# Kernel optimization log

Measured on AMD Instinct MI355X. Metric: run time of the kernel, lower is better.

Reference implementation:

```python
import jax, jax.numpy as jnp
import numpy as np

B, S, H, E, K, F = 2, 2048, 1024, 8, 2, 4096


def setup_inputs() -> dict:
    key = jax.random.key(0)
    ks = jax.random.split(key, 6)
    scale = 0.02
    return {
        "x": jax.random.normal(ks[0], (B, S, H), dtype=jnp.float32),
        "Wg": jax.random.normal(ks[1], (H, E), dtype=jnp.float32) * scale,
        "bg": jnp.zeros((E,), dtype=jnp.float32),
        "W1": jax.random.normal(ks[2], (E, H, F), dtype=jnp.float32) * scale,  # gate proj per expert
        "W3": jax.random.normal(ks[3], (E, H, F), dtype=jnp.float32) * scale,  # up proj per expert
        "W2": jax.random.normal(ks[4], (E, F, H), dtype=jnp.float32) * scale,  # down proj per expert
    }


def reference(x, Wg, bg, W1, W3, W2):
    # --- gating: softmax -> top-k -> renormalize ---
    probs = jax.nn.softmax(jnp.einsum("bsh,he->bse", x, Wg) + bg, axis=-1)  # [B,S,E]
    topw, topi = jax.lax.top_k(probs, K)                                     # [B,S,K]
    topw = topw / jnp.sum(topw, axis=-1, keepdims=True)
    # combine weights per expert: sum over k slots of weight where index==e
    cw = jnp.sum(jax.nn.one_hot(topi, E, dtype=x.dtype) * topw[..., None], axis=-2)  # [B,S,E]

    # --- dense grouped SwiGLU experts; cw==0 zeroes out non-selected tokens,
    # which is mathematically identical to the original masked gather/scatter loop ---
    g = jnp.einsum("bsh,ehf->bsef", x, W1)            # [B,S,E,F]
    u = jnp.einsum("bsh,ehf->bsef", x, W3)            # [B,S,E,F]
    h = jax.nn.silu(g) * u                             # [B,S,E,F]
    out = jnp.einsum("bsef,efh,bse->bsh", h, W2, cw)  # weighted combine
    return out
```

## Files before the change

kernel.cpp:

```cpp
#include <hip/hip_runtime.h>
#include <hip/hip_bf16.h>
#include <math.h>

#define HD 1024
#define FD 4096
#define NE 8
#define CAP 4096

typedef __attribute__((ext_vector_type(8))) short short8;
typedef __attribute__((ext_vector_type(4))) float f32x4;

__device__ inline unsigned short f2b(float f) {
    union { float f; unsigned u; } v; v.f = f;
    unsigned r = v.u + 0x7FFF + ((v.u >> 16) & 1);
    return (unsigned short)(r >> 16);
}

__device__ inline void gll16(const void* g, void* l) {
    __builtin_amdgcn_global_load_lds(
        (const __attribute__((address_space(1))) unsigned int*)g,
        (__attribute__((address_space(3))) unsigned int*)l, 16, 0, 0);
}

__global__ __launch_bounds__(256) void convx_kernel(const float* __restrict__ x,
                                                    unsigned short* __restrict__ xbf)
{
    int i = blockIdx.x * 256 + threadIdx.x;
    float4 v = *(const float4*)(x + (size_t)i * 4);
    ushort4 b; b.x = f2b(v.x); b.y = f2b(v.y); b.z = f2b(v.z); b.w = f2b(v.w);
    *(ushort4*)(xbf + (size_t)i * 4) = b;
}

__global__ __launch_bounds__(256) void transpose_kernel(const float* __restrict__ in,
                                                        unsigned short* __restrict__ out,
                                                        int R, int C)
{
    __shared__ unsigned short Ls[64 * 72];
    int t = threadIdx.x;
    int r0 = blockIdx.x * 64, c0 = blockIdx.y * 64;
    const float* ip = in + (size_t)blockIdx.z * R * C;
    unsigned short* op = out + (size_t)blockIdx.z * R * C;

    int rl = t >> 4, c4 = (t & 15) * 4;
#pragma unroll
    for (int p = 0; p < 4; p++) {
        int r = p * 16 + rl;
        float4 v = *(const float4*)(ip + (size_t)(r0 + r) * C + c0 + c4);
        Ls[(c4 + 0) * 72 + r] = f2b(v.x);
        Ls[(c4 + 1) * 72 + r] = f2b(v.y);
        Ls[(c4 + 2) * 72 + r] = f2b(v.z);
        Ls[(c4 + 3) * 72 + r] = f2b(v.w);
    }
    __syncthreads();
    int c = t >> 2, j2 = (t & 3) * 2;
#pragma unroll
    for (int q = 0; q < 2; q++) {
        int j = j2 + q;
        uint4 v = *(const uint4*)&Ls[c * 72 + j * 8];
        *(uint4*)(op + (size_t)(c0 + c) * R + r0 + j * 8) = v;
    }
}

__global__ __launch_bounds__(256) void gate_kernel(
    const float* __restrict__ x, const float* __restrict__ Wg,
    const float* __restrict__ bg, int* __restrict__ cnt,
    int* __restrict__ btok, float* __restrict__ bw,
    int* __restrict__ tokSlot, int T)
{
    int wave = threadIdx.x >> 6;
    int lane = threadIdx.x & 63;
    int t = blockIdx.x * 4 + wave;
    if (t >= T) return;

    float part[NE];
#pragma unroll
    for (int e = 0; e < NE; e++) part[e] = 0.f;
    const float* xr = x + (size_t)t * HD;
#pragma unroll 4
    for (int j = 0; j < 16; j++) {
        int h = lane + 64 * j;
        float xv = xr[h];
        const float* wr = Wg + h * NE;
#pragma unroll
        for (int e = 0; e < NE; e++) part[e] += xv * wr[e];
    }
#pragma unroll
    for (int e = 0; e < NE; e++) {
        float v = part[e];
        for (int off = 32; off >= 1; off >>= 1) v += __shfl_xor(v, off, 64);
        part[e] = v;
    }
    if (lane == 0) {
        float lg[NE];
#pragma unroll
        for (int e = 0; e < NE; e++) lg[e] = part[e] + bg[e];
        int i0 = 0;
        for (int e = 1; e < NE; e++) if (lg[e] > lg[i0]) i0 = e;
        int i1 = -1;
        for (int e = 0; e < NE; e++) {
            if (e == i0) continue;
            if (i1 < 0 || lg[e] > lg[i1]) i1 = e;
        }
        float e1 = expf(lg[i1] - lg[i0]);
        float s = 1.0f + e1;
        float w0 = 1.0f / s, w1 = e1 / s;
        int p0 = atomicAdd(&cnt[i0], 1);
        int p1 = atomicAdd(&cnt[i1], 1);
        btok[i0 * CAP + p0] = t; bw[i0 * CAP + p0] = w0;
        btok[i1 * CAP + p1] = t; bw[i1 * CAP + p1] = w1;
        tokSlot[t * 2 + 0] = i0 * CAP + p0;
        tokSlot[t * 2 + 1] = i1 * CAP + p1;
    }
}

__global__ void scan_kernel(const int* __restrict__ cnt, int* __restrict__ offs)
{
    if (threadIdx.x == 0) {
        int acc = 0;
        for (int e = 0; e < NE; e++) { offs[e] = acc; acc += cnt[e]; }
    }
}

__global__ __launch_bounds__(256, 2) void gemm1_kernel(
    const unsigned short* __restrict__ xbf, const unsigned short* __restrict__ Wt1,
    const unsigned short* __restrict__ Wt3, const int* __restrict__ btok,
    const int* __restrict__ cnt, const int* __restrict__ offs,
    unsigned short* __restrict__ h_buf)
{
    int e = blockIdx.z;
    int ne = cnt[e];
    int m0 = blockIdx.y * 128;
    if (m0 >= ne) return;
    int f0 = blockIdx.x * 128;

    __shared__ unsigned short As[3][4096];
    __shared__ unsigned short B1s[3][4096];
    __shared__ unsigned short B3s[3][4096];

    int tid = threadIdx.x;
    int lane = tid & 63;
    int w = tid >> 6;
    int wm = (w >> 1) * 64, wn = (w & 1) * 64;
    int l15 = lane & 15, quad = lane >> 4;

    const unsigned short* W1e = Wt1 + (size_t)e * HD * FD;
    const unsigned short* W3e = Wt3 + (size_t)e * HD * FD;

    const unsigned short* aA[2];
    const unsigned short* aB1[2];
    const unsigned short* aB3[2];
    int dst[2];
#pragma unroll
    for (int q = 0; q < 2; q++) {
        int row = q * 64 + lane;
        dst[q] = w * 1024 + q * 512;
        int ridx = m0 + row; if (ridx >= ne) ridx = ne - 1;
        int tok = btok[e * CAP + ridx];
        aA[q]  = xbf + (size_t)tok * HD + w * 8;
        aB1[q] = W1e + (size_t)(f0 + row) * HD + w * 8;
        aB3[q] = W3e + (size_t)(f0 + row) * HD + w * 8;
    }

    int aoff[4], boff[4];
#pragma unroll
    for (int i = 0; i < 4; i++) {
        aoff[i] = quad * 1024 + (wm + i * 16 + l15) * 8;
        boff[i] = quad * 1024 + (wn + i * 16 + l15) * 8;
    }

    f32x4 accG[4][4], accU[4][4];
    f32x4 z = {0.f, 0.f, 0.f, 0.f};
#pragma unroll
    for (int i = 0; i < 4; i++)
#pragma unroll
        for (int jj = 0; jj < 4; jj++) { accG[i][jj] = z; accU[i][jj] = z; }

#pragma unroll
    for (int q = 0; q < 2; q++) {
        gll16(aA[q],  &As[0][dst[q]]);
        gll16(aB1[q], &B1s[0][dst[q]]);
        gll16(aB3[q], &B3s[0][dst[q]]);
    }
#pragma unroll
    for (int q = 0; q < 2; q++) {
        gll16(aA[q]  + 32, &As[1][dst[q]]);
        gll16(aB1[q] + 32, &B1s[1][dst[q]]);
        gll16(aB3[q] + 32, &B3s[1][dst[q]]);
    }

    const int NK = HD / 32;
    int cur = 0;
    for (int k = 0; k < NK; ++k) {
        if (k + 2 < NK) {
            int nb = cur + 2; if (nb >= 3) nb -= 3;
            int k0 = (k + 2) * 32;
#pragma unroll
            for (int q = 0; q < 2; q++) {
                gll16(aA[q]  + k0, &As[nb][dst[q]]);
                gll16(aB1[q] + k0, &B1s[nb][dst[q]]);
                gll16(aB3[q] + k0, &B3s[nb][dst[q]]);
            }
            asm volatile("s_waitcnt vmcnt(12)\ns_barrier" ::: "memory");
        } else if (k + 1 < NK) {
            asm volatile("s_waitcnt vmcnt(6)\ns_barrier" ::: "memory");
        } else {
            asm volatile("s_waitcnt vmcnt(0)\ns_barrier" ::: "memory");
        }

        __builtin_amdgcn_s_setprio(1);
        short8 af[4], b1f[4], b3f[4];
#pragma unroll
        for (int mt = 0; mt < 4; mt++) af[mt] = *(const short8*)&As[cur][aoff[mt]];
#pragma unroll
        for (int nt = 0; nt < 4; nt++) {
            b1f[nt] = *(const short8*)&B1s[cur][boff[nt]];
            b3f[nt] = *(const short8*)&B3s[cur][boff[nt]];
        }
#pragma unroll
        for (int mt = 0; mt < 4; mt++)
#pragma unroll
            for (int nt = 0; nt < 4; nt++) {
                accG[mt][nt] = __builtin_amdgcn_mfma_f32_16x16x32_bf16(af[mt], b1f[nt], accG[mt][nt], 0, 0, 0);
                accU[mt][nt] = __builtin_amdgcn_mfma_f32_16x16x32_bf16(af[mt], b3f[nt], accU[mt][nt], 0, 0, 0);
            }
        __builtin_amdgcn_s_setprio(0);
        asm volatile("s_barrier" ::: "memory");
        cur++; if (cur >= 3) cur -= 3;
    }

    int base = offs[e] + m0;
#pragma unroll
    for (int mt = 0; mt < 4; mt++) {
#pragma unroll
        for (int r = 0; r < 4; r++) {
            int rowl = wm + mt * 16 + quad * 4 + r;
            if (m0 + rowl < ne) {
                size_t rb = (size_t)(base + rowl) * FD;
#pragma unroll
                for (int nt = 0; nt < 4; nt++) {
                    int f = f0 + wn + nt * 16 + l15;
                    float g = accG[mt][nt][r];
                    float u = accU[mt][nt][r];
                    float h = g / (1.f + expf(-g)) * u;
                    h_buf[rb + f] = f2b(h);
                }
            }
        }
    }
}

__global__ __launch_bounds__(256, 3) void gemm2_kernel(
    const unsigned short* __restrict__ h_buf, const unsigned short* __restrict__ Wt2,
    const float* __restrict__ bw, const int* __restrict__ cnt,
    const int* __restrict__ offs, float* __restrict__ contrib)
{
    int e = blockIdx.z;
    int ne = cnt[e];
    int m0 = blockIdx.y * 128;
    if (m0 >= ne) return;
    int h0 = blockIdx.x * 128;

    __shared__ unsigned short As[3][4096];
    __shared__ unsigned short Bs[3][4096];

    int tid = threadIdx.x;
    int lane = tid & 63;
    int w = tid >> 6;
    int wm = (w >> 1) * 64, wn = (w & 1) * 64;
    int l15 = lane & 15, quad = lane >> 4;
    int obase = offs[e];

    const unsigned short* W2e = Wt2 + (size_t)e * FD * HD;

    const unsigned short* aA[2];
    const unsigned short* aB[2];
    int dst[2];
#pragma unroll
    for (int q = 0; q < 2; q++) {
        int row = q * 64 + lane;
        dst[q] = w * 1024 + q * 512;
        int ridx = m0 + row; if (ridx >= ne) ridx = ne - 1;
        aA[q] = h_buf + (size_t)(obase + ridx) * FD + w * 8;
        aB[q] = W2e + (size_t)(h0 + row) * FD + w * 8;
    }

    int aoff[4], boff[4];
#pragma unroll
    for (int i = 0; i < 4; i++) {
        aoff[i] = quad * 1024 + (wm + i * 16 + l15) * 8;
        boff[i] = quad * 1024 + (wn + i * 16 + l15) * 8;
    }

    f32x4 acc[4][4];
    f32x4 z = {0.f, 0.f, 0.f, 0.f};
#pragma unroll
    for (int i = 0; i < 4; i++)
#pragma unroll
        for (int jj = 0; jj < 4; jj++) acc[i][jj] = z;

#pragma unroll
    for (int q = 0; q < 2; q++) {
        gll16(aA[q], &As[0][dst[q]]);
        gll16(aB[q], &Bs[0][dst[q]]);
    }
#pragma unroll
    for (int q = 0; q < 2; q++) {
        gll16(aA[q] + 32, &As[1][dst[q]]);
        gll16(aB[q] + 32, &Bs[1][dst[q]]);
    }

    const int NK = FD / 32;
    int cur = 0;
    for (int k = 0; k < NK; ++k) {
        if (k + 2 < NK) {
            int nb = cur + 2; if (nb >= 3) nb -= 3;
            int k0 = (k + 2) * 32;
#pragma unroll
            for (int q = 0; q < 2; q++) {
                gll16(aA[q] + k0, &As[nb][dst[q]]);
                gll16(aB[q] + k0, &Bs[nb][dst[q]]);
            }
            asm volatile("s_waitcnt vmcnt(8)\ns_barrier" ::: "memory");
        } else if (k + 1 < NK) {
            asm volatile("s_waitcnt vmcnt(4)\ns_barrier" ::: "memory");
        } else {
            asm volatile("s_waitcnt vmcnt(0)\ns_barrier" ::: "memory");
        }

        __builtin_amdgcn_s_setprio(1);
        short8 af[4], bf[4];
#pragma unroll
        for (int mt = 0; mt < 4; mt++) af[mt] = *(const short8*)&As[cur][aoff[mt]];
#pragma unroll
        for (int nt = 0; nt < 4; nt++) bf[nt] = *(const short8*)&Bs[cur][boff[nt]];
#pragma unroll
        for (int mt = 0; mt < 4; mt++)
#pragma unroll
            for (int nt = 0; nt < 4; nt++)
                acc[mt][nt] = __builtin_amdgcn_mfma_f32_16x16x32_bf16(af[mt], bf[nt], acc[mt][nt], 0, 0, 0);
        __builtin_amdgcn_s_setprio(0);
        asm volatile("s_barrier" ::: "memory");
        cur++; if (cur >= 3) cur -= 3;
    }

    int base = obase + m0;
#pragma unroll
    for (int mt = 0; mt < 4; mt++) {
#pragma unroll
        for (int r = 0; r < 4; r++) {
            int rowl = wm + mt * 16 + quad * 4 + r;
            if (m0 + rowl < ne) {
                float wgt = bw[e * CAP + m0 + rowl];
                size_t rb = (size_t)(base + rowl) * HD;
#pragma unroll
                for (int nt = 0; nt < 4; nt++) {
                    int col = h0 + wn + nt * 16 + l15;
                    contrib[rb + col] = acc[mt][nt][r] * wgt;
                }
            }
        }
    }
}

__global__ __launch_bounds__(256) void combine_kernel(
    const float* __restrict__ contrib, const int* __restrict__ tokSlot,
    const int* __restrict__ offs, float* __restrict__ out)
{
    int t = blockIdx.x;
    int i = threadIdx.x;
    int s0 = tokSlot[t * 2 + 0];
    int s1 = tokSlot[t * 2 + 1];
    int r0 = offs[s0 >> 12] + (s0 & (CAP - 1));
    int r1 = offs[s1 >> 12] + (s1 & (CAP - 1));
    float4 a = *(const float4*)(contrib + (size_t)r0 * HD + i * 4);
    float4 b = *(const float4*)(contrib + (size_t)r1 * HD + i * 4);
    float4 o;
    o.x = a.x + b.x; o.y = a.y + b.y; o.z = a.z + b.z; o.w = a.w + b.w;
    *(float4*)(out + (size_t)t * HD + i * 4) = o;
}

extern "C" void kernel_launch(void* const* d_in, const int* in_sizes, int n_in,
                              void* d_out, int out_size, void* d_ws, size_t ws_size,
                              hipStream_t stream)
{
    const float* x  = (const float*)d_in[0];
    const float* Wg = (const float*)d_in[1];
    const float* bg = (const float*)d_in[2];
    const float* W1 = (const float*)d_in[3];
    const float* W3 = (const float*)d_in[4];
    const float* W2 = (const float*)d_in[5];
    float* out = (float*)d_out;
    int T = in_sizes[0] / HD;

    char* ws = (char*)d_ws;
    int*   cnt     = (int*)ws;
    int*   offs    = cnt + 8;
    int*   btok    = (int*)(ws + 1024);
    float* bw      = (float*)(ws + 1024 + 131072);
    int*   tokSlot = (int*)(ws + 1024 + 262144);
    unsigned short* xbf = (unsigned short*)(ws + ((size_t)1 << 20));
    unsigned short* Wt1 = (unsigned short*)(ws + ((size_t)16 << 20));
    unsigned short* Wt3 = (unsigned short*)(ws + ((size_t)80 << 20));
    unsigned short* Wt2 = (unsigned short*)(ws + ((size_t)144 << 20));
    unsigned short* h_buf = (unsigned short*)(ws + ((size_t)208 << 20));
    float* contrib = (float*)(ws + ((size_t)272 << 20));

    hipMemsetAsync(cnt, 0, 8 * sizeof(int), stream);

    convx_kernel<<<(T * HD) / 1024, 256, 0, stream>>>(x, xbf);
    dim3 tg1(HD / 64, FD / 64, NE);
    transpose_kernel<<<tg1, 256, 0, stream>>>(W1, Wt1, HD, FD);
    transpose_kernel<<<tg1, 256, 0, stream>>>(W3, Wt3, HD, FD);
    dim3 tg2(FD / 64, HD / 64, NE);
    transpose_kernel<<<tg2, 256, 0, stream>>>(W2, Wt2, FD, HD);

    gate_kernel<<<(T + 3) / 4, 256, 0, stream>>>(x, Wg, bg, cnt, btok, bw, tokSlot, T);
    scan_kernel<<<1, 64, 0, stream>>>(cnt, offs);

    dim3 g1(FD / 128, CAP / 128, NE);
    gemm1_kernel<<<g1, 256, 0, stream>>>(xbf, Wt1, Wt3, btok, cnt, offs, h_buf);

    dim3 g2(HD / 128, CAP / 128, NE);
    gemm2_kernel<<<g2, 256, 0, stream>>>(h_buf, Wt2, bw, cnt, offs, contrib);

    combine_kernel<<<T, 256, 0, stream>>>(contrib, tokSlot, offs, out);
}
```

Baseline: 1.012 ms.

## Pre-tile transposed expert weights into contiguous 128x32 k-blocks and use row-major LDS tiles

The weight transpose kernel now writes bf16 weights in a blocked layout where each 128-row output block is stored as consecutive 128x32 k-slices. The GEMM kernels can then fetch a whole B tile as one contiguous 8KB chunk per k-step instead of 128 strided 64-byte row pieces. A-tile loads are also rearranged so each row's 32 k-elements are split across 4 adjacent lanes, with matching row-major LDS fragment offsets. This is meant to improve global-load coalescing and DRAM locality for the weight streams. The row-major LDS layout with a 64-byte row stride may introduce more bank conflicts on fragment reads.

```diff
diff --git a/kernel.cpp b/kernel.cpp
--- a/kernel.cpp
+++ b/kernel.cpp
@@ -39,7 +39,7 @@
     int t = threadIdx.x;
     int r0 = blockIdx.x * 64, c0 = blockIdx.y * 64;
     const float* ip = in + (size_t)blockIdx.z * R * C;
-    unsigned short* op = out + (size_t)blockIdx.z * R * C;
+    unsigned short* op = out + (size_t)blockIdx.z * (size_t)R * C;
 
     int rl = t >> 4, c4 = (t & 15) * 4;
 #pragma unroll
@@ -53,11 +53,15 @@
     }
     __syncthreads();
     int c = t >> 2, j2 = (t & 3) * 2;
+    int orow = c0 + c;
+    int blk = orow >> 7, rl2 = orow & 127;
 #pragma unroll
     for (int q = 0; q < 2; q++) {
         int j = j2 + q;
+        int kk = r0 + j * 8;
         uint4 v = *(const uint4*)&Ls[c * 72 + j * 8];
-        *(uint4*)(op + (size_t)(c0 + c) * R + r0 + j * 8) = v;
+        size_t dst = (size_t)blk * 128 * R + (size_t)(kk >> 5) * 4096 + rl2 * 32 + (kk & 31);
+        *(uint4*)(op + dst) = v;
     }
 }
 
@@ -143,8 +147,8 @@
     int wm = (w >> 1) * 64, wn = (w & 1) * 64;
     int l15 = lane & 15, quad = lane >> 4;
 
-    const unsigned short* W1e = Wt1 + (size_t)e * HD * FD;
-    const unsigned short* W3e = Wt3 + (size_t)e * HD * FD;
+    const unsigned short* W1e = Wt1 + (size_t)e * HD * FD + (size_t)blockIdx.x * (128 * HD);
+    const unsigned short* W3e = Wt3 + (size_t)e * HD * FD + (size_t)blockIdx.x * (128 * HD);
 
     const unsigned short* aA[2];
     const unsigned short* aB1[2];
@@ -152,20 +156,22 @@
     int dst[2];
 #pragma unroll
     for (int q = 0; q < 2; q++) {
-        int row = q * 64 + lane;
-        dst[q] = w * 1024 + q * 512;
+        int g = w * 2 + q;
+        int row = g * 16 + (lane >> 2);
+        int cofs = (lane & 3) * 8;
+        dst[q] = g * 512;
         int ridx = m0 + row; if (ridx >= ne) ridx = ne - 1;
         int tok = btok[e * CAP + ridx];
-        aA[q]  = xbf + (size_t)tok * HD + w * 8;
-        aB1[q] = W1e + (size_t)(f0 + row) * HD + w * 8;
-        aB3[q] = W3e + (size_t)(f0 + row) * HD + w * 8;
+        aA[q]  = xbf + (size_t)tok * HD + cofs;
+        aB1[q] = W1e + g * 512 + lane * 8;
+        aB3[q] = W3e + g * 512 + lane * 8;
     }
 
     int aoff[4], boff[4];
 #pragma unroll
     for (int i = 0; i < 4; i++) {
-        aoff[i] = quad * 1024 + (wm + i * 16 + l15) * 8;
-        boff[i] = quad * 1024 + (wn + i * 16 + l15) * 8;
+        aoff[i] = (wm + i * 16 + l15) * 32 + quad * 8;
+        boff[i] = (wn + i * 16 + l15) * 32 + quad * 8;
     }
 
     f32x4 accG[4][4], accU[4][4];
@@ -183,9 +189,9 @@
     }
 #pragma unroll
     for (int q = 0; q < 2; q++) {
-        gll16(aA[q]  + 32, &As[1][dst[q]]);
-        gll16(aB1[q] + 32, &B1s[1][dst[q]]);
-        gll16(aB3[q] + 32, &B3s[1][dst[q]]);
+        gll16(aA[q]  + 32,   &As[1][dst[q]]);
+        gll16(aB1[q] + 4096, &B1s[1][dst[q]]);
+        gll16(aB3[q] + 4096, &B3s[1][dst[q]]);
     }
 
     const int NK = HD / 32;
@@ -193,12 +199,11 @@
     for (int k = 0; k < NK; ++k) {
         if (k + 2 < NK) {
             int nb = cur + 2; if (nb >= 3) nb -= 3;
-            int k0 = (k + 2) * 32;
 #pragma unroll
             for (int q = 0; q < 2; q++) {
-                gll16(aA[q]  + k0, &As[nb][dst[q]]);
-                gll16(aB1[q] + k0, &B1s[nb][dst[q]]);
-                gll16(aB3[q] + k0, &B3s[nb][dst[q]]);
+                gll16(aA[q]  + (k + 2) * 32,            &As[nb][dst[q]]);
+                gll16(aB1[q] + (size_t)(k + 2) * 4096,  &B1s[nb][dst[q]]);
+                gll16(aB3[q] + (size_t)(k + 2) * 4096,  &B3s[nb][dst[q]]);
             }
             asm volatile("s_waitcnt vmcnt(12)\ns_barrier" ::: "memory");
         } else if (k + 1 < NK) {
@@ -270,25 +275,27 @@
     int l15 = lane & 15, quad = lane >> 4;
     int obase = offs[e];
 
-    const unsigned short* W2e = Wt2 + (size_t)e * FD * HD;
+    const unsigned short* W2e = Wt2 + (size_t)e * FD * HD + (size_t)blockIdx.x * (128 * FD);
 
     const unsigned short* aA[2];
     const unsigned short* aB[2];
     int dst[2];
 #pragma unroll
     for (int q = 0; q < 2; q++) {
-        int row = q * 64 + lane;
-        dst[q] = w * 1024 + q * 512;
+        int g = w * 2 + q;
+        int row = g * 16 + (lane >> 2);
+        int cofs = (lane & 3) * 8;
+        dst[q] = g * 512;
         int ridx = m0 + row; if (ridx >= ne) ridx = ne - 1;
-        aA[q] = h_buf + (size_t)(obase + ridx) * FD + w * 8;
-        aB[q] = W2e + (size_t)(h0 + row) * FD + w * 8;
+        aA[q] = h_buf + (size_t)(obase + ridx) * FD + cofs;
+        aB[q] = W2e + g * 512 + lane * 8;
     }
 
     int aoff[4], boff[4];
 #pragma unroll
     for (int i = 0; i < 4; i++) {
-        aoff[i] = quad * 1024 + (wm + i * 16 + l15) * 8;
-        boff[i] = quad * 1024 + (wn + i * 16 + l15) * 8;
+        aoff[i] = (wm + i * 16 + l15) * 32 + quad * 8;
+        boff[i] = (wn + i * 16 + l15) * 32 + quad * 8;
     }
 
     f32x4 acc[4][4];
@@ -305,8 +312,8 @@
     }
 #pragma unroll
     for (int q = 0; q < 2; q++) {
-        gll16(aA[q] + 32, &As[1][dst[q]]);
-        gll16(aB[q] + 32, &Bs[1][dst[q]]);
+        gll16(aA[q] + 32,   &As[1][dst[q]]);
+        gll16(aB[q] + 4096, &Bs[1][dst[q]]);
     }
 
     const int NK = FD / 32;
@@ -314,11 +321,10 @@
     for (int k = 0; k < NK; ++k) {
         if (k + 2 < NK) {
             int nb = cur + 2; if (nb >= 3) nb -= 3;
-            int k0 = (k + 2) * 32;
 #pragma unroll
             for (int q = 0; q < 2; q++) {
-                gll16(aA[q] + k0, &As[nb][dst[q]]);
-                gll16(aB[q] + k0, &Bs[nb][dst[q]]);
+                gll16(aA[q] + (k + 2) * 32,           &As[nb][dst[q]]);
+                gll16(aB[q] + (size_t)(k + 2) * 4096, &Bs[nb][dst[q]]);
             }
             asm volatile("s_waitcnt vmcnt(8)\ns_barrier" ::: "memory");
         } else if (k + 1 < NK) {
```

Result: faster. 865.9 us (-14.4%).
